# Kernel tuning notes

Hardware: AMD Instinct MI355X
Metric: run time of the kernel (lower is better)

The kernel has to match this reference:

```python
import jax, jax.numpy as jnp
import numpy as np

EPS = 1e-5  # torch InstanceNorm2d default
C = 512

def setup_inputs() -> dict:
    key = jax.random.key(0)
    ks = jax.random.split(key, 9)
    x = jax.random.normal(ks[0], (4, C, 64, 64), dtype=jnp.float32)
    s = 0.05
    wq = jax.random.normal(ks[1], (C, C), dtype=jnp.float32) * s
    wk = jax.random.normal(ks[2], (C, C), dtype=jnp.float32) * s
    wv = jax.random.normal(ks[3], (C, C), dtype=jnp.float32) * s
    wp = jax.random.normal(ks[4], (C, C), dtype=jnp.float32) * s
    bq = jax.random.normal(ks[5], (C,), dtype=jnp.float32) * s
    bk = jax.random.normal(ks[6], (C,), dtype=jnp.float32) * s
    bv = jax.random.normal(ks[7], (C,), dtype=jnp.float32) * s
    bp = jax.random.normal(ks[8], (C,), dtype=jnp.float32) * s
    return {"x": x, "wq": wq, "bq": bq, "wk": wk, "bk": bk,
            "wv": wv, "bv": bv, "wp": wp, "bp": bp}

def _conv1x1(h, w, b):
    # 1x1 conv == per-pixel channel mixing: (b,c,h,w) x (o,c) -> (b,o,h,w)
    return jnp.einsum('bchw,oc->bohw', h, w) + b[None, :, None, None]

def reference(x, wq, bq, wk, bk, wv, bv, wp, bp):
    b, c, h, w = x.shape
    # InstanceNorm2d (affine=False): normalize each (b,c) plane over spatial dims
    mu = jnp.mean(x, axis=(2, 3), keepdims=True)
    var = jnp.mean(jnp.square(x - mu), axis=(2, 3), keepdims=True)
    hn = (x - mu) * jax.lax.rsqrt(var + EPS)
    q = _conv1x1(hn, wq, bq).reshape(b, c, h * w)
    k = _conv1x1(hn, wk, bk).reshape(b, c, h * w)
    v = _conv1x1(hn, wv, bv).reshape(b, c, h * w)
    # attn[b,i,j] = <q[:, i], k[:, j]> / sqrt(c), softmax over keys j
    attn = jnp.einsum('bci,bcj->bij', q, k) / jnp.sqrt(jnp.asarray(c, x.dtype))
    attn = jax.nn.softmax(attn, axis=2)
    # out[b,c,i] = sum_j v[b,c,j] * attn[b,i,j]
    o = jnp.einsum('bcj,bij->bci', v, attn).reshape(b, c, h, w)
    return x + _conv1x1(o, wp, bp)
```

## Files before the change

kernel.cpp:

```cpp
#include <hip/hip_runtime.h>
#include <hip/hip_bf16.h>

typedef short bf16x8 __attribute__((ext_vector_type(8)));
typedef float f32x4 __attribute__((ext_vector_type(4)));

#define CCH 512
#define NPIX 4096
#define NB 4

__device__ inline unsigned short f2bf(float f) {
  union { __hip_bfloat16 h; unsigned short u; } cv;
  cv.h = __float2bfloat16(f);
  return cv.u;
}

#define GLD16(gp, lp) __builtin_amdgcn_global_load_lds( \
    (const __attribute__((address_space(1))) unsigned int*)(gp), \
    (__attribute__((address_space(3))) unsigned int*)(lp), 16, 0, 0)

__global__ __launch_bounds__(256) void cast_weights_k(
    const float* __restrict__ w0, const float* __restrict__ w1,
    const float* __restrict__ w2, const float* __restrict__ w3,
    unsigned short* __restrict__ out) {
  int z = blockIdx.y;
  const float* src = (z == 0) ? w0 : (z == 1) ? w1 : (z == 2) ? w2 : w3;
  long i = (long)blockIdx.x * 256 + threadIdx.x;
  out[(long)z * CCH * CCH + i] = f2bf(src[i]);
}

__global__ __launch_bounds__(256) void bias_concat_k(
    const float* __restrict__ bq, const float* __restrict__ bk,
    float* __restrict__ bqk) {
  int i = blockIdx.x * 256 + threadIdx.x;
  bqk[i] = (i < CCH) ? bq[i] : bk[i - CCH];
}

__global__ __launch_bounds__(256) void zero_l_k(float* __restrict__ lsum) {
  int i = (blockIdx.x * 256 + threadIdx.x) * 4;
  *(float4*)(lsum + i) = make_float4(0.f, 0.f, 0.f, 0.f);
}

__global__ __launch_bounds__(256) void stats_k(const float* __restrict__ x,
                                               float* __restrict__ stats) {
  long plane = blockIdx.x;
  const float4* p = (const float4*)(x + plane * NPIX);
  int t = threadIdx.x;
  float s = 0.f, q = 0.f;
  for (int c = 0; c < 4; c++) {
    float4 v = p[c * 256 + t];
    s += v.x + v.y + v.z + v.w;
    q += v.x * v.x + v.y * v.y + v.z * v.z + v.w * v.w;
  }
  for (int off = 32; off; off >>= 1) { s += __shfl_xor(s, off); q += __shfl_xor(q, off); }
  __shared__ float rs[4], rq[4];
  int w = t >> 6;
  if ((t & 63) == 0) { rs[w] = s; rq[w] = q; }
  __syncthreads();
  if (t == 0) {
    s = rs[0] + rs[1] + rs[2] + rs[3];
    q = rq[0] + rq[1] + rq[2] + rq[3];
    float mu = s * (1.f / NPIX);
    float var = q * (1.f / NPIX) - mu * mu;
    stats[2 * plane] = mu;
    stats[2 * plane + 1] = rsqrtf(var + 1e-5f);
  }
}

__global__ __launch_bounds__(256) void norm_t_k(const float* __restrict__ x,
                                                const float* __restrict__ stats,
                                                unsigned short* __restrict__ hnT) {
  int b = blockIdx.z;
  int c0 = blockIdx.y * 32, i0 = blockIdx.x * 32;
  __shared__ float tile[32][33];
  int t = threadIdx.x;
  int il = t & 31, cl = t >> 5;
  for (int r = 0; r < 4; r++) {
    int c = c0 + cl + r * 8;
    long pl = (long)b * CCH + c;
    float mu = stats[2 * pl], rsg = stats[2 * pl + 1];
    tile[cl + r * 8][il] = (x[pl * NPIX + i0 + il] - mu) * rsg;
  }
  __syncthreads();
  for (int r = 0; r < 4; r++) {
    int i = i0 + cl + r * 8;
    hnT[((long)b * NPIX + i) * CCH + c0 + il] = f2bf(tile[il][cl + r * 8]);
  }
}

#define SH(sl, ha, h, kt) do {                                               \
    const unsigned short* g_ = ((ha) ? gB : gA) + (long)(kt) * 64 +          \
                               (long)(2 * (h)) * 65536;                      \
    char* l_ = (char*)LDSu + (sl) * 65536 + (ha) * 32768 + (2 * (h)) * 8192  \
               + t * 16;                                                     \
    GLD16(g_, l_);                                                           \
    GLD16(g_ + 65536, l_ + 8192);                                            \
  } while (0)

#define READ_A(sl, half) do {                                                \
    const unsigned short* sa_ = LDSu + (sl) * 32768;                         \
    _Pragma("unroll") for (int mm = 0; mm < 4; mm++) {                       \
      int row = ((half) * 4 + mm) * 32 + wr * 16 + fr;                       \
      a_[mm][0] = *(const bf16x8*)(sa_ + row * 64 + o0_);                    \
      a_[mm][1] = *(const bf16x8*)(sa_ + row * 64 + o1_);                    \
    }                                                                        \
  } while (0)

#define READ_B(sl, half, dst) do {                                           \
    const unsigned short* sb_ = LDSu + (sl) * 32768 + 16384;                 \
    _Pragma("unroll") for (int nn = 0; nn < 2; nn++) {                       \
      int row = ((half) * 2 + nn) * 64 + wc * 16 + fr;                       \
      dst[nn][0] = *(const bf16x8*)(sb_ + row * 64 + o0_);                   \
      dst[nn][1] = *(const bf16x8*)(sb_ + row * 64 + o1_);                   \
    }                                                                        \
  } while (0)

#define MF(qm, qn, bb)                                                       \
    _Pragma("unroll") for (int mm = 0; mm < 4; mm++)                         \
      _Pragma("unroll") for (int nn = 0; nn < 2; nn++) {                     \
        acc[(qm) * 4 + mm][(qn) * 2 + nn] =                                  \
            __builtin_amdgcn_mfma_f32_16x16x32_bf16(                         \
                a_[mm][0], bb[nn][0], acc[(qm) * 4 + mm][(qn) * 2 + nn],     \
                0, 0, 0);                                                    \
        acc[(qm) * 4 + mm][(qn) * 2 + nn] =                                  \
            __builtin_amdgcn_mfma_f32_16x16x32_bf16(                         \
                a_[mm][1], bb[nn][1], acc[(qm) * 4 + mm][(qn) * 2 + nn],     \
                0, 0, 0);                                                    \
      }

#define PHASE(VN, SSTMT, RSTMT, MSTMT) do {                                  \
    SSTMT;                                                                   \
    RSTMT;                                                                   \
    if ((VN) == 8) asm volatile("s_waitcnt vmcnt(8)" ::: "memory");          \
    else if ((VN) == 0) asm volatile("s_waitcnt vmcnt(0)" ::: "memory");     \
    __builtin_amdgcn_s_barrier();                                            \
    asm volatile("s_waitcnt lgkmcnt(0)" ::: "memory");                       \
    __builtin_amdgcn_sched_barrier(0);                                       \
    __builtin_amdgcn_s_setprio(1);                                           \
    MSTMT;                                                                   \
    __builtin_amdgcn_s_setprio(0);                                           \
    __builtin_amdgcn_sched_barrier(0);                                       \
    __builtin_amdgcn_s_barrier();                                            \
  } while (0)

#define GROUP_S(sl, tn)                                                      \
    PHASE(-1, (void)0, { READ_A(sl, 0); READ_B(sl, 0, b0_); }, MF(0, 0, b0_)); \
    PHASE(-1, { SH(sl, 0, 0, tn); SH(sl, 1, 0, tn); },                       \
          READ_B(sl, 1, b1_), MF(0, 1, b1_));                                \
    PHASE(-1, SH(sl, 1, 1, tn), READ_A(sl, 1), MF(1, 1, b1_));               \
    PHASE(8, SH(sl, 0, 1, tn), (void)0, MF(1, 0, b0_))

#define GROUP_N(sl, VN3)                                                     \
    PHASE(-1, (void)0, { READ_A(sl, 0); READ_B(sl, 0, b0_); }, MF(0, 0, b0_)); \
    PHASE(-1, (void)0, READ_B(sl, 1, b1_), MF(0, 1, b1_));                   \
    PHASE(-1, (void)0, READ_A(sl, 1), MF(1, 1, b1_));                        \
    PHASE(VN3, (void)0, (void)0, MF(1, 0, b0_))

__global__ __launch_bounds__(512, 2) void gemm8p_s_k(
    const unsigned short* __restrict__ A,
    const unsigned short* __restrict__ B,
    unsigned short* __restrict__ C,
    float* __restrict__ lsum, float scale) {
  const int z = blockIdx.z;
  const long SLAB2 = (long)NPIX * 1024;
  const long SLABP = (long)NPIX * NPIX;
  A += z * SLAB2;
  B += z * SLAB2;
  const int m0 = blockIdx.y * 256, n0 = blockIdx.x * 256;
  const int t = threadIdx.x;
  const int lane = t & 63, w = t >> 6;
  const int wr = w >> 2, wc = w & 3;
  const int fr = lane & 15, fq = lane >> 4;
  const int chx = fr & 7;
  const int o0_ = (fq ^ chx) * 8, o1_ = ((fq + 4) ^ chx) * 8;

  __shared__ __align__(16) unsigned short LDSu[2 * 32768];

  f32x4 acc[8][4] = {};
  bf16x8 a_[4][2], b0_[2][2], b1_[2][2];

  const int srow = t >> 3;
  const int scol = ((t & 7) ^ (srow & 7)) * 8;
  const unsigned short* gA = A + (long)(m0 + srow) * 1024 + scol;
  const unsigned short* gB = B + (long)(n0 + srow) * 1024 + scol;

  SH(0, 0, 0, 0); SH(0, 1, 0, 0); SH(0, 0, 1, 0); SH(0, 1, 1, 0);
  SH(1, 0, 0, 1); SH(1, 1, 0, 1); SH(1, 0, 1, 1); SH(1, 1, 1, 1);
  asm volatile("s_waitcnt vmcnt(8)" ::: "memory");
  __builtin_amdgcn_s_barrier();

  GROUP_S(0, 2); GROUP_S(1, 3);
  GROUP_S(0, 4); GROUP_S(1, 5);
  GROUP_S(0, 6); GROUP_S(1, 7);
  GROUP_N(0, 0);
  GROUP_N(1, -1);

  float rsum[8][4];
  for (int i = 0; i < 8; i++)
    for (int r = 0; r < 4; r++) rsum[i][r] = 0.f;
  for (int i = 0; i < 8; i++) {
    int mg = m0 + i * 32 + wr * 16 + fq * 4;
    for (int j = 0; j < 4; j++) {
      int ng = n0 + j * 64 + wc * 16 + fr;
      for (int r = 0; r < 4; r++) {
        float v = exp2f(acc[i][j][r] * scale);
        rsum[i][r] += v;
        C[z * SLABP + (long)(mg + r) * 4096 + ng] = f2bf(v);
      }
    }
  }
  for (int i = 0; i < 8; i++)
    for (int r = 0; r < 4; r++) {
      float s = rsum[i][r];
      s += __shfl_xor(s, 1);
      s += __shfl_xor(s, 2);
      s += __shfl_xor(s, 4);
      s += __shfl_xor(s, 8);
      if (fr == 0)
        atomicAdd(&lsum[z * NPIX + m0 + i * 32 + wr * 16 + fq * 4 + r], s);
    }
}
#undef SH
#undef READ_A
#undef READ_B
#undef MF
#undef PHASE
#undef GROUP_S
#undef GROUP_N

template <int XCDX, int OUTF32, int BIASM, bool RESID, bool SCALE, bool EXPSUM, bool ROWSCALE>
__global__ __launch_bounds__(256) void gemm_bt_k(
    const unsigned short* __restrict__ A, const unsigned short* __restrict__ B,
    void* __restrict__ Cv, const float* __restrict__ bias,
    const float* __restrict__ resid, float* __restrict__ lsum,
    int K, int lda, int ldb, int ldc,
    long sA, long sB, long sC, float scale) {
  int z = blockIdx.z;
  A += z * sA;
  B += z * sB;

  int bx = blockIdx.x, by = blockIdx.y;
  if (XCDX > 0) {
    int s = blockIdx.x + gridDim.x * blockIdx.y;
    int xcd = s & 7, idx = s >> 3;
    int rw = gridDim.x / XCDX;
    int rh = (gridDim.y * XCDX) >> 3;
    int rx0 = (xcd % XCDX) * rw, ry0 = (xcd / XCDX) * rh;
    bx = rx0 + idx % rw;
    by = ry0 + idx / rw;
  }
  const int n0 = bx * 128, m0 = by * 128;

  const int t = threadIdx.x;
  const int lane = t & 63, w = t >> 6;
  const int wr = w >> 1, wc = w & 1;

  __shared__ __align__(16) unsigned short As[128 * 64];
  __shared__ __align__(16) unsigned short Bs[128 * 64];

  f32x4 acc[4][4] = {};

  const int srow = t >> 3;
  const int scol = (((t & 7) ^ (srow & 7)) * 8);
  const unsigned short* ga = A + (long)(m0 + srow) * lda + scol;
  const unsigned short* gb = B + (long)(n0 + srow) * ldb + scol;
  char* lA = (char*)As + t * 16;
  char* lB = (char*)Bs + t * 16;
  const long stpa = (long)32 * lda;
  const long stpb = (long)32 * ldb;

  const int fr = lane & 15, fq = lane >> 4;
  const int chx = fr & 7;
  const unsigned short* rA = As + (wr * 64 + fr) * 64;
  const unsigned short* rB = Bs + (wc * 64 + fr) * 64;

  const int nkt = K >> 6;
  for (int kt = 0; kt < nkt; kt++) {
    const unsigned short* gak = ga + (long)kt * 64;
    const unsigned short* gbk = gb + (long)kt * 64;
    GLD16(gak, lA);
    GLD16(gak + stpa, lA + 4096);
    GLD16(gak + 2 * stpa, lA + 8192);
    GLD16(gak + 3 * stpa, lA + 12288);
    GLD16(gbk, lB);
    GLD16(gbk + stpb, lB + 4096);
    GLD16(gbk + 2 * stpb, lB + 8192);
    GLD16(gbk + 3 * stpb, lB + 12288);
    __syncthreads();
    for (int kk = 0; kk < 2; kk++) {
      const int offA = ((fq + kk * 4) ^ chx) * 8;
      bf16x8 af[4], bfr[4];
      for (int i = 0; i < 4; i++) af[i] = *(const bf16x8*)(rA + i * 1024 + offA);
      for (int i = 0; i < 4; i++) bfr[i] = *(const bf16x8*)(rB + i * 1024 + offA);
      for (int i = 0; i < 4; i++)
        for (int j = 0; j < 4; j++)
          acc[i][j] = __builtin_amdgcn_mfma_f32_16x16x32_bf16(af[i], bfr[j], acc[i][j], 0, 0, 0);
    }
    __syncthreads();
  }

  if (OUTF32) {
    float* Cf = (float*)Cv;
    for (int i = 0; i < 4; i++) {
      int mg = m0 + wr * 64 + i * 16 + fq * 4;
      for (int j = 0; j < 4; j++) {
        int ng = n0 + wc * 64 + j * 16 + fr;
        for (int r = 0; r < 4; r++) {
          float v = acc[i][j][r];
          if (SCALE) v *= scale;
          int m = mg + r;
          if (BIASM == 1) v += bias[m];
          else if (BIASM == 2) v += bias[ng];
          long off = z * sC + (long)m * ldc + ng;
          if (RESID) v += resid[off];
          Cf[off] = v;
        }
      }
    }
  } else {
    float linv[4][4];
    if (ROWSCALE) {
      for (int i = 0; i < 4; i++)
        for (int r = 0; r < 4; r++)
          linv[i][r] = 1.f / lsum[z * NPIX + m0 + wr * 64 + i * 16 + fq * 4 + r];
    }
    float rsum[4][4];
    if (EXPSUM) {
      for (int i = 0; i < 4; i++)
        for (int r = 0; r < 4; r++) rsum[i][r] = 0.f;
    }
    unsigned short* Cb = (unsigned short*)Cv;
    for (int i = 0; i < 4; i++) {
      int mg = m0 + wr * 64 + i * 16 + fq * 4;
      for (int j = 0; j < 4; j++) {
        int ng = n0 + wc * 64 + j * 16 + fr;
        for (int r = 0; r < 4; r++) {
          float v = acc[i][j][r];
          if (SCALE) v *= scale;
          if (BIASM == 1) v += bias[mg + r];
          else if (BIASM == 2) v += bias[ng];
          if (EXPSUM) { v = exp2f(v); rsum[i][r] += v; }
          if (ROWSCALE) v *= linv[i][r];
          Cb[z * sC + (long)(mg + r) * ldc + ng] = f2bf(v);
        }
      }
    }
    if (EXPSUM) {
      for (int i = 0; i < 4; i++)
        for (int r = 0; r < 4; r++) {
          float s = rsum[i][r];
          s += __shfl_xor(s, 1);
          s += __shfl_xor(s, 2);
          s += __shfl_xor(s, 4);
          s += __shfl_xor(s, 8);
          if (fr == 0)
            atomicAdd(&lsum[z * NPIX + m0 + wr * 64 + i * 16 + fq * 4 + r], s);
        }
    }
  }
}

extern "C" void kernel_launch(void* const* d_in, const int* in_sizes, int n_in,
                              void* d_out, int out_size, void* d_ws, size_t ws_size,
                              hipStream_t stream) {
  const float* x  = (const float*)d_in[0];
  const float* wq = (const float*)d_in[1];
  const float* bq = (const float*)d_in[2];
  const float* wk = (const float*)d_in[3];
  const float* bk = (const float*)d_in[4];
  const float* wv = (const float*)d_in[5];
  const float* bv = (const float*)d_in[6];
  const float* wp = (const float*)d_in[7];
  const float* bp = (const float*)d_in[8];

  char* ws = (char*)d_ws;
  const long SLAB = (long)NPIX * CCH;
  const long SLAB2 = (long)NPIX * 1024;
  const long SLABP = (long)NPIX * NPIX;

  float* stats = (float*)ws;
  float* bqk = (float*)(ws + (32l << 10));
  float* lsum = (float*)(ws + (64l << 10));
  unsigned short* wbf = (unsigned short*)(ws + (192l << 10));
  unsigned short* hnT = (unsigned short*)(ws + (192l << 10) + (1l << 21));
  unsigned short* QKt = hnT + 4 * SLAB;
  unsigned short* V   = QKt + 4 * SLAB2;
  unsigned short* Ot  = V + 4 * SLAB;
  unsigned short* S4  = Ot + 4 * SLAB;

  unsigned short* wv_bf = wbf + 2 * 262144;
  unsigned short* wp_bf = wbf + 3 * 262144;

  cast_weights_k<<<dim3(1024, 4, 1), 256, 0, stream>>>(wq, wk, wv, wp, wbf);
  bias_concat_k<<<dim3(4, 1, 1), 256, 0, stream>>>(bq, bk, bqk);
  zero_l_k<<<dim3(16, 1, 1), 256, 0, stream>>>(lsum);
  stats_k<<<dim3(NB * CCH, 1, 1), 256, 0, stream>>>(x, stats);
  norm_t_k<<<dim3(128, 16, 4), 256, 0, stream>>>(x, stats, hnT);

  gemm_bt_k<1, 0, 2, false, false, false, false><<<dim3(8, 32, 4), 256, 0, stream>>>(
      hnT, wbf, QKt, bqk, nullptr, nullptr, 512, 512, 512, 1024, SLAB, 0, SLAB2, 1.f);
  gemm_bt_k<2, 0, 1, false, false, false, false><<<dim3(32, 4, 4), 256, 0, stream>>>(
      wv_bf, hnT, V, bv, nullptr, nullptr, 512, 512, 512, 4096, 0, SLAB, SLAB, 1.f);

  const float isc2 = 0.06375871387551278f;
  gemm8p_s_k<<<dim3(16, 16, 4), 512, 0, stream>>>(QKt, QKt + 512, S4, lsum, isc2);
  gemm_bt_k<1, 0, 0, false, false, false, true><<<dim3(4, 32, 4), 256, 0, stream>>>(
      S4, V, Ot, nullptr, nullptr, lsum, 4096, 4096, 4096, 512, SLABP, SLAB, SLAB, 1.f);
  gemm_bt_k<2, 1, 1, true, false, false, false><<<dim3(32, 4, 4), 256, 0, stream>>>(
      wp_bf, Ot, d_out, bp, x, nullptr, 512, 512, 512, 4096, 0, SLAB, SLAB, 1.f);
}
```

Baseline: 294.0 us.

## Make score GEMM blocks loop over four N tiles with cross-tile prefetch

Each workgroup of the QK^T score kernel now computes four consecutive 256-wide column tiles instead of one, with the grid shrunk from 16x16x4 to 4x16x4. The next tile's first K slabs are prefetched during the current tile's last groups, so the pipeline does not drain and refill between tiles. Blocks are also remapped so each XCD handles contiguous row bands, improving L2 reuse of the A operand. The trade-off is fewer workgroups (256 total, about one wave per CU at 2 blocks/CU) and a longer serial epilogue per block, since the exp/store/atomic epilogue is not overlapped with loads.

```diff
diff --git a/kernel.cpp b/kernel.cpp
--- a/kernel.cpp
+++ b/kernel.cpp
@@ -87,8 +87,8 @@
   }
 }
 
-#define SH(sl, ha, h, kt) do {                                               \
-    const unsigned short* g_ = ((ha) ? gB : gA) + (long)(kt) * 64 +          \
+#define SHT(sl, ha, h, kk, gBp) do {                                         \
+    const unsigned short* g_ = ((ha) ? (gBp) : gA) + (long)(kk) * 64 +       \
                                (long)(2 * (h)) * 65536;                      \
     char* l_ = (char*)LDSu + (sl) * 65536 + (ha) * 32768 + (2 * (h)) * 8192  \
                + t * 16;                                                     \
@@ -142,12 +142,12 @@
     __builtin_amdgcn_s_barrier();                                            \
   } while (0)
 
-#define GROUP_S(sl, tn)                                                      \
+#define GROUP_S(sl, kk, gBp)                                                 \
     PHASE(-1, (void)0, { READ_A(sl, 0); READ_B(sl, 0, b0_); }, MF(0, 0, b0_)); \
-    PHASE(-1, { SH(sl, 0, 0, tn); SH(sl, 1, 0, tn); },                       \
+    PHASE(-1, { SHT(sl, 0, 0, kk, gBp); SHT(sl, 1, 0, kk, gBp); },           \
           READ_B(sl, 1, b1_), MF(0, 1, b1_));                                \
-    PHASE(-1, SH(sl, 1, 1, tn), READ_A(sl, 1), MF(1, 1, b1_));               \
-    PHASE(8, SH(sl, 0, 1, tn), (void)0, MF(1, 0, b0_))
+    PHASE(-1, SHT(sl, 1, 1, kk, gBp), READ_A(sl, 1), MF(1, 1, b1_));         \
+    PHASE(8, SHT(sl, 0, 1, kk, gBp), (void)0, MF(1, 0, b0_))
 
 #define GROUP_N(sl, VN3)                                                     \
     PHASE(-1, (void)0, { READ_A(sl, 0); READ_B(sl, 0, b0_); }, MF(0, 0, b0_)); \
@@ -165,7 +165,10 @@
   const long SLABP = (long)NPIX * NPIX;
   A += z * SLAB2;
   B += z * SLAB2;
-  const int m0 = blockIdx.y * 256, n0 = blockIdx.x * 256;
+  int s = blockIdx.x + 4 * blockIdx.y;
+  int xcd = s & 7, idx = s >> 3;
+  int bx = idx & 3, by = xcd * 2 + (idx >> 2);
+  const int m0 = by * 256, n0b = bx * 1024;
   const int t = threadIdx.x;
   const int lane = t & 63, w = t >> 6;
   const int wr = w >> 2, wc = w & 3;
@@ -181,45 +184,61 @@
   const int srow = t >> 3;
   const int scol = ((t & 7) ^ (srow & 7)) * 8;
   const unsigned short* gA = A + (long)(m0 + srow) * 1024 + scol;
-  const unsigned short* gB = B + (long)(n0 + srow) * 1024 + scol;
-
-  SH(0, 0, 0, 0); SH(0, 1, 0, 0); SH(0, 0, 1, 0); SH(0, 1, 1, 0);
-  SH(1, 0, 0, 1); SH(1, 1, 0, 1); SH(1, 0, 1, 1); SH(1, 1, 1, 1);
+  const unsigned short* gB = B + (long)(n0b + srow) * 1024 + scol;
+  const long BSTR = (long)256 * 1024;
+
+  SHT(0, 0, 0, 0, gB); SHT(0, 1, 0, 0, gB); SHT(0, 0, 1, 0, gB); SHT(0, 1, 1, 0, gB);
+  SHT(1, 0, 0, 1, gB); SHT(1, 1, 0, 1, gB); SHT(1, 0, 1, 1, gB); SHT(1, 1, 1, 1, gB);
   asm volatile("s_waitcnt vmcnt(8)" ::: "memory");
   __builtin_amdgcn_s_barrier();
 
-  GROUP_S(0, 2); GROUP_S(1, 3);
-  GROUP_S(0, 4); GROUP_S(1, 5);
-  GROUP_S(0, 6); GROUP_S(1, 7);
-  GROUP_N(0, 0);
-  GROUP_N(1, -1);
-
-  float rsum[8][4];
-  for (int i = 0; i < 8; i++)
-    for (int r = 0; r < 4; r++) rsum[i][r] = 0.f;
-  for (int i = 0; i < 8; i++) {
-    int mg = m0 + i * 32 + wr * 16 + fq * 4;
-    for (int j = 0; j < 4; j++) {
-      int ng = n0 + j * 64 + wc * 16 + fr;
+  for (int tt = 0; tt < 4; ++tt) {
+    const unsigned short* gBc = gB + (long)tt * BSTR;
+    if (tt < 3) {
+      const unsigned short* gBn = gBc + BSTR;
+      GROUP_S(0, 2, gBc); GROUP_S(1, 3, gBc);
+      GROUP_S(0, 4, gBc); GROUP_S(1, 5, gBc);
+      GROUP_S(0, 6, gBc); GROUP_S(1, 7, gBc);
+      GROUP_S(0, 0, gBn); GROUP_S(1, 1, gBn);
+    } else {
+      GROUP_S(0, 2, gBc); GROUP_S(1, 3, gBc);
+      GROUP_S(0, 4, gBc); GROUP_S(1, 5, gBc);
+      GROUP_S(0, 6, gBc); GROUP_S(1, 7, gBc);
+      GROUP_N(0, 0); GROUP_N(1, -1);
+    }
+    const int n0 = n0b + tt * 256;
+    float rsum[8][4];
+    for (int i = 0; i < 8; i++)
+      for (int r = 0; r < 4; r++) rsum[i][r] = 0.f;
+    for (int i = 0; i < 8; i++) {
+      int mg = m0 + i * 32 + wr * 16 + fq * 4;
+      for (int j = 0; j < 4; j++) {
+        int ng = n0 + j * 64 + wc * 16 + fr;
+        for (int r = 0; r < 4; r++) {
+          float v = exp2f(acc[i][j][r] * scale);
+          rsum[i][r] += v;
+          C[z * SLABP + (long)(mg + r) * 4096 + ng] = f2bf(v);
+        }
+      }
+    }
+    for (int i = 0; i < 8; i++)
       for (int r = 0; r < 4; r++) {
-        float v = exp2f(acc[i][j][r] * scale);
-        rsum[i][r] += v;
-        C[z * SLABP + (long)(mg + r) * 4096 + ng] = f2bf(v);
+        float ss = rsum[i][r];
+        ss += __shfl_xor(ss, 1);
+        ss += __shfl_xor(ss, 2);
+        ss += __shfl_xor(ss, 4);
+        ss += __shfl_xor(ss, 8);
+        if (fr == 0)
+          atomicAdd(&lsum[z * NPIX + m0 + i * 32 + wr * 16 + fq * 4 + r], ss);
       }
-    }
-  }
-  for (int i = 0; i < 8; i++)
-    for (int r = 0; r < 4; r++) {
-      float s = rsum[i][r];
-      s += __shfl_xor(s, 1);
-      s += __shfl_xor(s, 2);
-      s += __shfl_xor(s, 4);
-      s += __shfl_xor(s, 8);
-      if (fr == 0)
-        atomicAdd(&lsum[z * NPIX + m0 + i * 32 + wr * 16 + fq * 4 + r], s);
-    }
-}
-#undef SH
+    if (tt < 3) {
+      f32x4 zz = {0.f, 0.f, 0.f, 0.f};
+      for (int i = 0; i < 8; i++)
+        for (int j = 0; j < 4; j++) acc[i][j] = zz;
+    }
+  }
+}
+#undef SHT
 #undef READ_A
 #undef READ_B
 #undef MF
@@ -402,7 +421,7 @@
       wv_bf, hnT, V, bv, nullptr, nullptr, 512, 512, 512, 4096, 0, SLAB, SLAB, 1.f);
 
   const float isc2 = 0.06375871387551278f;
-  gemm8p_s_k<<<dim3(16, 16, 4), 512, 0, stream>>>(QKt, QKt + 512, S4, lsum, isc2);
+  gemm8p_s_k<<<dim3(4, 16, 4), 512, 0, stream>>>(QKt, QKt + 512, S4, lsum, isc2);
   gemm_bt_k<1, 0, 0, false, false, false, true><<<dim3(4, 32, 4), 256, 0, stream>>>(
       S4, V, Ot, nullptr, nullptr, lsum, 4096, 4096, 4096, 512, SLABP, SLAB, SLAB, 1.f);
   gemm_bt_k<2, 1, 1, true, false, false, false><<<dim3(32, 4, 4), 256, 0, stream>>>(
```

Measured after the change: 636.8 us. 2.17x slower.

## Add 8-wave pipelined PV GEMM kernel with async LDS loads and row scaling

Applied to the files above, without the earlier changes.

Replaces the generic gemm_bt_k used for the P·V product with a dedicated 512-thread kernel using 256x128 tiles. It double-buffers K-slices in swizzled LDS via global_load_lds, interleaves loads, LDS reads and MFMA in barrier-separated phases with raised scheduling priority, and applies the 1/lsum softmax normalization in the epilogue. The aim is to keep the matrix units busy on the largest GEMM, at the cost of more LDS per block and a hand-tuned schedule that is fixed to these shapes.

```diff
diff --git a/kernel.cpp b/kernel.cpp
--- a/kernel.cpp
+++ b/kernel.cpp
@@ -226,6 +226,140 @@
 #undef PHASE
 #undef GROUP_S
 #undef GROUP_N
+
+#define SH_A(sl, h, kk) do {                                                 \
+    const unsigned short* g_ = gA + (long)(kk) * 64 + (long)(2 * (h)) * 262144; \
+    char* l_ = (char*)LDSu + (sl) * 32768 + (2 * (h)) * 8192 + t * 16;       \
+    GLD16(g_, l_);                                                           \
+    GLD16(g_ + 262144, l_ + 8192);                                           \
+  } while (0)
+
+#define SH_B(sl, h, kk) do {                                                 \
+    const unsigned short* g_ = gB + (long)(kk) * 64 + (long)(h) * 262144;    \
+    char* l_ = (char*)LDSu + 65536 + (sl) * 16384 + (h) * 8192 + t * 16;     \
+    GLD16(g_, l_);                                                           \
+  } while (0)
+
+#define READ_PA(sl, half) do {                                               \
+    const unsigned short* sa_ = LDSu + (sl) * 16384;                         \
+    _Pragma("unroll") for (int mm = 0; mm < 2; mm++) {                       \
+      int row = ((half) * 2 + mm) * 64 + wr * 16 + fr;                       \
+      a_[mm][0] = *(const bf16x8*)(sa_ + row * 64 + o0_);                    \
+      a_[mm][1] = *(const bf16x8*)(sa_ + row * 64 + o1_);                    \
+    }                                                                        \
+  } while (0)
+
+#define READ_PB(sl, half, dst) do {                                          \
+    const unsigned short* sb_ = LDSu + 32768 + (sl) * 8192;                  \
+    _Pragma("unroll") for (int nn = 0; nn < 2; nn++) {                       \
+      int row = ((half) * 2 + nn) * 32 + wc * 16 + fr;                       \
+      dst[nn][0] = *(const bf16x8*)(sb_ + row * 64 + o0_);                   \
+      dst[nn][1] = *(const bf16x8*)(sb_ + row * 64 + o1_);                   \
+    }                                                                        \
+  } while (0)
+
+#define MF_P(qm, qn, bb)                                                     \
+    _Pragma("unroll") for (int mm = 0; mm < 2; mm++)                         \
+      _Pragma("unroll") for (int nn = 0; nn < 2; nn++) {                     \
+        acc[(qm) * 2 + mm][(qn) * 2 + nn] =                                  \
+            __builtin_amdgcn_mfma_f32_16x16x32_bf16(                         \
+                a_[mm][0], bb[nn][0], acc[(qm) * 2 + mm][(qn) * 2 + nn],     \
+                0, 0, 0);                                                    \
+        acc[(qm) * 2 + mm][(qn) * 2 + nn] =                                  \
+            __builtin_amdgcn_mfma_f32_16x16x32_bf16(                         \
+                a_[mm][1], bb[nn][1], acc[(qm) * 2 + mm][(qn) * 2 + nn],     \
+                0, 0, 0);                                                    \
+      }
+
+#define PHP(VN, SSTMT, RSTMT, MSTMT) do {                                    \
+    SSTMT;                                                                   \
+    RSTMT;                                                                   \
+    if ((VN) == 6) asm volatile("s_waitcnt vmcnt(6)" ::: "memory");          \
+    else if ((VN) == 0) asm volatile("s_waitcnt vmcnt(0)" ::: "memory");     \
+    __builtin_amdgcn_s_barrier();                                            \
+    asm volatile("s_waitcnt lgkmcnt(0)" ::: "memory");                       \
+    __builtin_amdgcn_sched_barrier(0);                                       \
+    __builtin_amdgcn_s_setprio(1);                                           \
+    MSTMT;                                                                   \
+    __builtin_amdgcn_s_setprio(0);                                           \
+    __builtin_amdgcn_sched_barrier(0);                                       \
+    __builtin_amdgcn_s_barrier();                                            \
+  } while (0)
+
+#define GROUP_PS(sl, kk)                                                     \
+    PHP(-1, (void)0, { READ_PA(sl, 0); READ_PB(sl, 0, b0_); }, MF_P(0, 0, b0_)); \
+    PHP(-1, { SH_A(sl, 0, kk); SH_B(sl, 0, kk); },                           \
+        READ_PB(sl, 1, b1_), MF_P(0, 1, b1_));                               \
+    PHP(-1, SH_B(sl, 1, kk), READ_PA(sl, 1), MF_P(1, 1, b1_));               \
+    PHP(6, SH_A(sl, 1, kk), (void)0, MF_P(1, 0, b0_))
+
+#define GROUP_PN(sl, VN3)                                                    \
+    PHP(-1, (void)0, { READ_PA(sl, 0); READ_PB(sl, 0, b0_); }, MF_P(0, 0, b0_)); \
+    PHP(-1, (void)0, READ_PB(sl, 1, b1_), MF_P(0, 1, b1_));                  \
+    PHP(-1, (void)0, READ_PA(sl, 1), MF_P(1, 1, b1_));                       \
+    PHP(VN3, (void)0, (void)0, MF_P(1, 0, b0_))
+
+__global__ __launch_bounds__(512, 2) void gemm8p_pv_k(
+    const unsigned short* __restrict__ A,
+    const unsigned short* __restrict__ B,
+    unsigned short* __restrict__ C,
+    const float* __restrict__ lsum) {
+  const int z = blockIdx.z;
+  const long SLAB = (long)NPIX * CCH;
+  const long SLABP = (long)NPIX * NPIX;
+  A += z * SLABP;
+  B += z * SLAB;
+  const int m0 = blockIdx.y * 256, n0 = blockIdx.x * 128;
+  const int t = threadIdx.x;
+  const int lane = t & 63, w = t >> 6;
+  const int wr = w >> 1, wc = w & 1;
+  const int fr = lane & 15, fq = lane >> 4;
+  const int chx = fr & 7;
+  const int o0_ = (fq ^ chx) * 8, o1_ = ((fq + 4) ^ chx) * 8;
+
+  __shared__ __align__(16) unsigned short LDSu[49152];
+
+  f32x4 acc[4][4] = {};
+  bf16x8 a_[2][2], b0_[2][2], b1_[2][2];
+
+  const int srow = t >> 3;
+  const int scol = ((t & 7) ^ (srow & 7)) * 8;
+  const unsigned short* gA = A + (long)(m0 + srow) * 4096 + scol;
+  const unsigned short* gB = B + (long)(n0 + srow) * 4096 + scol;
+
+  SH_A(0, 0, 0); SH_B(0, 0, 0); SH_B(0, 1, 0); SH_A(0, 1, 0);
+  SH_A(1, 0, 1); SH_B(1, 0, 1); SH_B(1, 1, 1); SH_A(1, 1, 1);
+  asm volatile("s_waitcnt vmcnt(6)" ::: "memory");
+  __builtin_amdgcn_s_barrier();
+
+  for (int g = 0; g < 31; g++) {
+    GROUP_PS(0, 2 * g + 2);
+    GROUP_PS(1, 2 * g + 3);
+  }
+  GROUP_PN(0, 0);
+  GROUP_PN(1, -1);
+
+  float linv[4][4];
+  for (int i = 0; i < 4; i++)
+    for (int r = 0; r < 4; r++)
+      linv[i][r] = 1.f / lsum[z * NPIX + m0 + i * 64 + wr * 16 + fq * 4 + r];
+  for (int i = 0; i < 4; i++) {
+    int mg = m0 + i * 64 + wr * 16 + fq * 4;
+    for (int j = 0; j < 4; j++) {
+      int ng = n0 + j * 32 + wc * 16 + fr;
+      for (int r = 0; r < 4; r++)
+        C[z * SLAB + (long)(mg + r) * 512 + ng] = f2bf(acc[i][j][r] * linv[i][r]);
+    }
+  }
+}
+#undef SH_A
+#undef SH_B
+#undef READ_PA
+#undef READ_PB
+#undef MF_P
+#undef PHP
+#undef GROUP_PS
+#undef GROUP_PN
 
 template <int XCDX, int OUTF32, int BIASM, bool RESID, bool SCALE, bool EXPSUM, bool ROWSCALE>
 __global__ __launch_bounds__(256) void gemm_bt_k(
@@ -403,8 +537,7 @@
 
   const float isc2 = 0.06375871387551278f;
   gemm8p_s_k<<<dim3(16, 16, 4), 512, 0, stream>>>(QKt, QKt + 512, S4, lsum, isc2);
-  gemm_bt_k<1, 0, 0, false, false, false, true><<<dim3(4, 32, 4), 256, 0, stream>>>(
-      S4, V, Ot, nullptr, nullptr, lsum, 4096, 4096, 4096, 512, SLABP, SLAB, SLAB, 1.f);
+  gemm8p_pv_k<<<dim3(4, 16, 4), 512, 0, stream>>>(S4, V, Ot, lsum);
   gemm_bt_k<2, 1, 1, true, false, false, false><<<dim3(32, 4, 4), 256, 0, stream>>>(
       wp_bf, Ot, d_out, bp, x, nullptr, 512, 512, 512, 4096, 0, SLAB, SLAB, 1.f);
 }
```

Result: no change. 294.1 us (+0.0%).
